# Kernel tuning notes

Measured on AMD Instinct MI355X. Metric: run time of the kernel, lower is better.

Reference implementation:

```python
import jax, jax.numpy as jnp
import numpy as np

N = 15872   # number of predictions (31 * 512)
D = 129     # 128 image features + 1 objectness score
H = 128     # block MLP hidden width
IN = 2 * D + 1  # neighbor feats + main feats + add_info (IoU)
NUM_BLOCKS = 2


def _lin(k, fi, fo):
    return jax.random.normal(k, (fi, fo), jnp.float32) / np.sqrt(fi).astype(np.float32)


def setup_inputs() -> dict:
    key = jax.random.key(0)
    ks = jax.random.split(key, 24)
    # ragged neighborhood structure: mean size 16, exactly E = 16*N edges
    sizes = (np.arange(N) % 31) + 1
    E = int(sizes.sum())  # 253952
    rng = np.random.default_rng(0)
    nbr_idx = rng.integers(0, N, size=E).astype(np.int32)
    self_idx = np.repeat(np.arange(N, dtype=np.int32), sizes)  # sorted segment ids

    inp = {
        "interpolated": jax.random.normal(ks[0], (N, D), jnp.float32),
        "add_info": jax.random.uniform(ks[1], (E, 1), dtype=jnp.float32),
        "neighborhood_sizes": jnp.asarray(sizes, jnp.int32),
        "neighborhoods_indexes": jnp.asarray(nbr_idx),
        "self_indexes": jnp.asarray(self_idx),
    }
    # two (block, output) model pairs
    inp["b0_W1"] = _lin(ks[2], IN, H); inp["b0_b1"] = jnp.zeros((H,), jnp.float32)
    inp["b0_W2"] = _lin(ks[3], H, H);  inp["b0_b2"] = jnp.zeros((H,), jnp.float32)
    inp["b0_Wo"] = _lin(ks[4], H, D); inp["b0_bo"] = jnp.zeros((D,), jnp.float32)
    inp["b1_W1"] = _lin(ks[5], IN, H); inp["b1_b1"] = jnp.zeros((H,), jnp.float32)
    inp["b1_W2"] = _lin(ks[6], H, H);  inp["b1_b2"] = jnp.zeros((H,), jnp.float32)
    inp["b1_Wo"] = _lin(ks[7], H, D); inp["b1_bo"] = jnp.zeros((D,), jnp.float32)
    # final layers: 129 -> 64 -> 1
    inp["f_W1"] = _lin(ks[8], D, 64); inp["f_b1"] = jnp.zeros((64,), jnp.float32)
    inp["f_W2"] = _lin(ks[9], 64, 1); inp["f_b2"] = jnp.zeros((1,), jnp.float32)
    return inp


def _lnms_forward(interpolated, add_info, params, nbr_idx, self_idx):
    # params: list of (W1, b1, W2, b2, Wo, bo) per block, plus (fW1, fb1, fW2, fb2)
    for (W1, b1, W2, b2, Wo, bo) in params[:-1]:
        nbr = interpolated[nbr_idx]    # (E, D) gather of neighbor representations
        main = interpolated[self_idx]  # (E, D) gather of owning prediction
        x = jnp.concatenate([nbr, main, add_info], axis=1)  # (E, 2D+1)
        h = jax.nn.relu(x @ W1 + b1)
        h = jax.nn.relu(h @ W2 + b2)   # (E, H) processed neighborhoods
        # ragged per-neighborhood max pool (segments are contiguous/sorted)
        pooled = jax.ops.segment_max(h, self_idx, num_segments=N,
                                     indices_are_sorted=True)  # (N, H)
        block_output = pooled @ Wo + bo  # (N, D)
        interpolated = interpolated + block_output  # residual scatter-update
    fW1, fb1, fW2, fb2 = params[-1]
    return jax.nn.relu(interpolated @ fW1 + fb1) @ fW2 + fb2  # (N, 1)


def reference(interpolated, add_info,
              b0_W1, b0_b1, b0_W2, b0_b2, b0_Wo, b0_bo,
              b1_W1, b1_b1, b1_W2, b1_b2, b1_Wo, b1_bo,
              f_W1, f_b1, f_W2, f_b2,
              neighborhood_sizes, neighborhoods_indexes, self_indexes):
    params = [
        (b0_W1, b0_b1, b0_W2, b0_b2, b0_Wo, b0_bo),
        (b1_W1, b1_b1, b1_W2, b1_b2, b1_Wo, b1_bo),
        (f_W1, f_b1, f_W2, f_b2),
    ]
    return _lnms_forward(interpolated, add_info, params,
                         neighborhoods_indexes, self_indexes)
```

## Files before the change

### kernel.cpp

```cpp
#include <hip/hip_runtime.h>

#define NSEG 15872
#define DD 129
#define HH 128
#define NTILE (NSEG / 16)

typedef __attribute__((ext_vector_type(8))) short s16x8;
typedef __attribute__((ext_vector_type(4))) float f32x4;

__device__ __forceinline__ unsigned short f2bf(float x) {
  union { float f; unsigned u; } c; c.f = x;
  unsigned r = c.u + 0x7FFFu + ((c.u >> 16) & 1u);
  return (unsigned short)(r >> 16);
}

__global__ __launch_bounds__(256) void scan_sort_kernel(
    const int* __restrict__ sizes, int* __restrict__ offs,
    int* __restrict__ sorted) {
  extern __shared__ int dynS[];
  int* szS = dynS;
  int* tmpS = dynS + NSEG;
  __shared__ int sums[256];
  __shared__ int bins[1024];
  const int t = threadIdx.x;

  for (int i = t; i < NSEG; i += 256) szS[i] = sizes[i];
  for (int i = t; i < 1024; i += 256) bins[i] = 0;
  __syncthreads();

  const int chunk = (NSEG + 255) >> 8;
  const int s0 = t * chunk, s1 = min(s0 + chunk, NSEG);
  int s = 0;
  for (int i = s0; i < s1; ++i) s += szS[i];
  sums[t] = s;
  __syncthreads();
  for (int d = 1; d < 256; d <<= 1) {
    int u = (t >= d) ? sums[t - d] : 0;
    __syncthreads();
    sums[t] += u;
    __syncthreads();
  }
  int a = sums[t] - s;
  for (int i = s0; i < s1; ++i) { tmpS[i] = a; a += szS[i]; }
  __syncthreads();
  for (int i = t; i < NSEG; i += 256) offs[i] = tmpS[i];
  if (t == 255) offs[NSEG] = a;

  for (int i = t; i < NSEG; i += 256) {
    int sz = szS[i]; sz = sz < 0 ? 0 : (sz > 1023 ? 1023 : sz);
    atomicAdd(&bins[sz], 1);
  }
  __syncthreads();
  const int c0 = bins[t * 4], c1 = bins[t * 4 + 1];
  const int c2 = bins[t * 4 + 2], c3 = bins[t * 4 + 3];
  const int loc = c0 + c1 + c2 + c3;
  sums[t] = loc;
  __syncthreads();
  for (int d = 1; d < 256; d <<= 1) {
    int u = (t >= d) ? sums[t - d] : 0;
    __syncthreads();
    sums[t] += u;
    __syncthreads();
  }
  const int base = sums[t] - loc;
  bins[t * 4]     = base;
  bins[t * 4 + 1] = base + c0;
  bins[t * 4 + 2] = base + c0 + c1;
  bins[t * 4 + 3] = base + c0 + c1 + c2;
  __syncthreads();
  for (int i = t; i < NSEG; i += 256) {
    int sz = szS[i]; sz = sz < 0 ? 0 : (sz > 1023 ? 1023 : sz);
    int pos = atomicAdd(&bins[sz], 1);
    tmpS[pos] = i;
  }
  __syncthreads();
  for (int i = t; i < NSEG; i += 256) sorted[i] = tmpS[i];
}

__device__ __forceinline__ void packB8(short* out, int idx8, const float* W,
                                       int N, int ld, int ncols, int kLimit,
                                       int rowBase) {
  const int n = (idx8 >> 3) % N;
  const int g = idx8 / (8 * N);
  s16x8 o;
#pragma unroll
  for (int i = 0; i < 8; ++i) {
    const int row = g * 8 + i;
    float v = 0.f;
    if (row < kLimit && n < ncols) v = W[(long)(rowBase + row) * ld + n];
    o[i] = (short)f2bf(v);
  }
  *(s16x8*)(out + idx8) = o;
}

__device__ __forceinline__ void packB2perm8(short* out, int idx8,
                                            const float* W) {
  const int n = (idx8 >> 3) & 127;
  const int g = idx8 >> 10;
  s16x8 o;
#pragma unroll
  for (int i = 0; i < 8; ++i)
    o[i] = (short)f2bf(W[(long)(i * 16 + g) * HH + n]);
  *(s16x8*)(out + idx8) = o;
}

#define PACK_IDS 161792
#define TAB_IDS (NSEG * 160)
#define PACKV (PACK_IDS / 8)
#define TABV (TAB_IDS / 8)
__global__ __launch_bounds__(256) void pack_tab_kernel(
    const float* __restrict__ interp, unsigned short* __restrict__ tab,
    const float* __restrict__ W1b0, const float* __restrict__ W1b1,
    const float* __restrict__ W2b0, const float* __restrict__ W2b1,
    const float* __restrict__ Wob0, const float* __restrict__ Wob1,
    const float* __restrict__ fW1, short* __restrict__ PB1,
    short* __restrict__ PB2, short* __restrict__ PWo,
    short* __restrict__ PW1m, short* __restrict__ PfW1) {
  int vid = blockIdx.x * 256 + threadIdx.x;
  if (vid < PACKV) {
    int idx = vid * 8;
    if (idx < 40960) {
      packB8(PB1 + (idx / 20480) * 20480, idx % 20480,
             (idx < 20480) ? W1b0 : W1b1, 128, 128, 128, 129, 0);
      return;
    }
    idx -= 40960;
    if (idx < 32768) {
      packB2perm8(PB2 + (idx / 16384) * 16384, idx % 16384,
                  (idx < 16384) ? W2b0 : W2b1);
      return;
    }
    idx -= 32768;
    if (idx < 36864) {
      packB8(PWo + (idx / 18432) * 18432, idx % 18432,
             (idx < 18432) ? Wob0 : Wob1, 144, 129, 129, 128, 0);
      return;
    }
    idx -= 36864;
    if (idx < 40960) {
      packB8(PW1m + (idx / 20480) * 20480, idx % 20480,
             (idx < 20480) ? W1b0 : W1b1, 128, 128, 128, 129, 129);
      return;
    }
    idx -= 40960;
    packB8(PfW1, idx, fW1, 64, 64, 64, 129, 0);
    return;
  }
  vid -= PACKV;
  if (vid < TABV) {
    const int n = vid / 20;
    const int g = vid - n * 20;
    s16x8 o = (s16x8){0, 0, 0, 0, 0, 0, 0, 0};
    if (g < 16) {
      const float* src = interp + (long)n * DD + g * 8;
#pragma unroll
      for (int i = 0; i < 8; ++i) o[i] = (short)f2bf(src[i]);
    } else if (g == 16) {
      o[0] = (short)f2bf(interp[(long)n * DD + 128]);
    }
    *(s16x8*)(tab + (long)vid * 8) = o;
  }
}

__global__ __launch_bounds__(256) void hmprep_kernel(
    const unsigned short* __restrict__ tab, const short* __restrict__ PW1m,
    const float* __restrict__ b1, float* __restrict__ Hm) {
  const int lane = threadIdx.x & 63, w = threadIdx.x >> 6;
  const int lk = lane >> 4, n16 = lane & 15;
  const int tile = blockIdx.x * 4 + w;
  const unsigned short* arow = tab + (long)(tile * 16 + n16) * 160;
  s16x8 A[5];
#pragma unroll
  for (int ks = 0; ks < 5; ++ks) A[ks] = *(const s16x8*)(arow + ks * 32 + lk * 8);
  f32x4 C[8];
#pragma unroll
  for (int nf = 0; nf < 8; ++nf) C[nf] = (f32x4){0.f, 0.f, 0.f, 0.f};
#pragma unroll
  for (int ks = 0; ks < 5; ++ks)
#pragma unroll
    for (int nf = 0; nf < 8; ++nf) {
      const s16x8 b = *(const s16x8*)(PW1m + (((ks * 4 + lk) * 128) + nf * 16 + n16) * 8);
      C[nf] = __builtin_amdgcn_mfma_f32_16x16x32_bf16(A[ks], b, C[nf], 0, 0, 0);
    }
#pragma unroll
  for (int nf = 0; nf < 8; ++nf) {
    const float bv = b1[nf * 16 + n16];
#pragma unroll
    for (int r = 0; r < 4; ++r)
      Hm[(long)(tile * 16 + lk * 4 + r) * HH + nf * 16 + n16] = C[nf][r] + bv;
  }
}

__device__ __forceinline__ int pairEdge(int row, int oLo, int sLo, int oHi,
                                        int sHi) {
  int e = (row < sLo) ? (oLo + row) : (oHi + row - sLo);
  if (row >= sLo + sHi) e = oHi + sHi - 1;
  return e;
}

__global__ __launch_bounds__(512, 2) void edge_kernel(
    const unsigned short* __restrict__ tab, const short* __restrict__ PB1,
    const short* __restrict__ PB2, const float* __restrict__ W1,
    const float* __restrict__ Hm, const float* __restrict__ iou,
    const int* __restrict__ nbrIdx, const int* __restrict__ offs,
    const int* __restrict__ sorted, const float* __restrict__ b2,
    unsigned short* __restrict__ pooled) {
  extern __shared__ __align__(16) char smem[];
  short* Bs1 = (short*)smem;
  short* Bs2 = (short*)(smem + 40960);
  short* stAll = (short*)(smem + 73728);
  {
    const f32x4* s1 = (const f32x4*)PB1;
    f32x4* d1 = (f32x4*)Bs1;
    for (int i = threadIdx.x; i < 2560; i += 512) d1[i] = s1[i];
    const f32x4* s2 = (const f32x4*)PB2;
    f32x4* d2 = (f32x4*)Bs2;
    for (int i = threadIdx.x; i < 2048; i += 512) d2[i] = s2[i];
  }
  __syncthreads();

  const int lane = threadIdx.x & 63;
  const int w = threadIdx.x >> 6;
  const int lk = lane >> 4, n16 = lane & 15;
  short* stA = stAll + w * 2 * (16 * 136);
  short* stB = stA + 16 * 136;

  float wv[8], bv[8];
#pragma unroll
  for (int nf = 0; nf < 8; ++nf) {
    wv[nf] = W1[258 * HH + nf * 16 + n16];
    bv[nf] = b2[nf * 16 + n16];
  }

  const int wid = (blockIdx.x << 3) + w;
  const int nw = gridDim.x << 3;
  const int npairs = NSEG >> 1;

  for (int p = wid; p < npairs; p += 2 * nw) {
    const int pA = p;
    int pB = p + nw;
    if (pB >= npairs) pB = pA;
    const int segLoA = sorted[pA], segHiA = sorted[NSEG - 1 - pA];
    const int segLoB = sorted[pB], segHiB = sorted[NSEG - 1 - pB];
    const int oLoA = offs[segLoA], sLoA = offs[segLoA + 1] - oLoA;
    const int oHiA = offs[segHiA], sHiA = offs[segHiA + 1] - oHiA;
    const int oLoB = offs[segLoB], sLoB = offs[segLoB + 1] - oLoB;
    const int oHiB = offs[segHiB], sHiB = offs[segHiB + 1] - oHiB;
    const int nt = (max(sLoA + sHiA, sLoB + sHiB) + 15) >> 4;

    float hmLoA[8], hmHiA[8], hmLoB[8], hmHiB[8];
    float pmLoA[8], pmHiA[8], pmLoB[8], pmHiB[8];
#pragma unroll
    for (int nf = 0; nf < 8; ++nf) {
      const int col = nf * 16 + n16;
      hmLoA[nf] = Hm[(long)segLoA * HH + col];
      hmHiA[nf] = Hm[(long)segHiA * HH + col];
      hmLoB[nf] = Hm[(long)segLoB * HH + col];
      hmHiB[nf] = Hm[(long)segHiB * HH + col];
      pmLoA[nf] = 0.f; pmHiA[nf] = 0.f; pmLoB[nf] = 0.f; pmHiB[nf] = 0.f;
    }

    for (int t = 0; t < nt; ++t) {
      const int row16 = (t << 4) + n16;
      const int eA = pairEdge(row16, oLoA, sLoA, oHiA, sHiA);
      const int eB = pairEdge(row16, oLoB, sLoB, oHiB, sHiB);
      const unsigned short* rA = tab + (long)nbrIdx[eA] * 160;
      const unsigned short* rB = tab + (long)nbrIdx[eB] * 160;
      s16x8 AA[5], AB[5];
#pragma unroll
      for (int ks = 0; ks < 5; ++ks) {
        AA[ks] = *(const s16x8*)(rA + ks * 32 + lk * 8);
        AB[ks] = *(const s16x8*)(rB + ks * 32 + lk * 8);
      }
      float ioA[4], ioB[4];
#pragma unroll
      for (int r = 0; r < 4; ++r) {
        const int row = (t << 4) + lk * 4 + r;
        ioA[r] = iou[pairEdge(row, oLoA, sLoA, oHiA, sHiA)];
        ioB[r] = iou[pairEdge(row, oLoB, sLoB, oHiB, sHiB)];
      }
      f32x4 C1A[8], C1B[8];
#pragma unroll
      for (int nf = 0; nf < 8; ++nf) {
        C1A[nf] = (f32x4){0.f, 0.f, 0.f, 0.f};
        C1B[nf] = (f32x4){0.f, 0.f, 0.f, 0.f};
      }
#pragma unroll
      for (int ks = 0; ks < 5; ++ks)
#pragma unroll
        for (int nf = 0; nf < 8; ++nf) {
          const s16x8 b = *(const s16x8*)(Bs1 + (((ks * 4 + lk) * 128) + nf * 16 + n16) * 8);
          C1A[nf] = __builtin_amdgcn_mfma_f32_16x16x32_bf16(AA[ks], b, C1A[nf], 0, 0, 0);
          C1B[nf] = __builtin_amdgcn_mfma_f32_16x16x32_bf16(AB[ks], b, C1B[nf], 0, 0, 0);
        }
#pragma unroll
      for (int r = 0; r < 4; ++r) {
        const int row = (t << 4) + lk * 4 + r;
        const bool lA = row < sLoA, lB = row < sLoB;
        s16x8 oA, oB;
#pragma unroll
        for (int nf = 0; nf < 8; ++nf) {
          const float hA = lA ? hmLoA[nf] : hmHiA[nf];
          const float hB = lB ? hmLoB[nf] : hmHiB[nf];
          oA[nf] = (short)f2bf(fmaxf(C1A[nf][r] + ioA[r] * wv[nf] + hA, 0.f));
          oB[nf] = (short)f2bf(fmaxf(C1B[nf][r] + ioB[r] * wv[nf] + hB, 0.f));
        }
        *(s16x8*)(stA + (lk * 4 + r) * 136 + n16 * 8) = oA;
        *(s16x8*)(stB + (lk * 4 + r) * 136 + n16 * 8) = oB;
      }
      s16x8 A2A[4], A2B[4];
#pragma unroll
      for (int ks = 0; ks < 4; ++ks) {
        A2A[ks] = *(const s16x8*)(stA + n16 * 136 + ks * 32 + lk * 8);
        A2B[ks] = *(const s16x8*)(stB + n16 * 136 + ks * 32 + lk * 8);
      }
      f32x4 C2A[8], C2B[8];
#pragma unroll
      for (int nf = 0; nf < 8; ++nf) {
        C2A[nf] = (f32x4){0.f, 0.f, 0.f, 0.f};
        C2B[nf] = (f32x4){0.f, 0.f, 0.f, 0.f};
      }
#pragma unroll
      for (int ks = 0; ks < 4; ++ks)
#pragma unroll
        for (int nf = 0; nf < 8; ++nf) {
          const s16x8 b = *(const s16x8*)(Bs2 + (((ks * 4 + lk) * 128) + nf * 16 + n16) * 8);
          C2A[nf] = __builtin_amdgcn_mfma_f32_16x16x32_bf16(A2A[ks], b, C2A[nf], 0, 0, 0);
          C2B[nf] = __builtin_amdgcn_mfma_f32_16x16x32_bf16(A2B[ks], b, C2B[nf], 0, 0, 0);
        }
#pragma unroll
      for (int r = 0; r < 4; ++r) {
        const int row = (t << 4) + lk * 4 + r;
        const bool lA = row < sLoA, lB = row < sLoB;
#pragma unroll
        for (int nf = 0; nf < 8; ++nf) {
          const float vA = C2A[nf][r] + bv[nf];
          const float vB = C2B[nf][r] + bv[nf];
          if (lA) pmLoA[nf] = fmaxf(pmLoA[nf], vA);
          else    pmHiA[nf] = fmaxf(pmHiA[nf], vA);
          if (lB) pmLoB[nf] = fmaxf(pmLoB[nf], vB);
          else    pmHiB[nf] = fmaxf(pmHiB[nf], vB);
        }
      }
    }
#pragma unroll
    for (int nf = 0; nf < 8; ++nf) {
      float a = pmLoA[nf], b = pmHiA[nf], c = pmLoB[nf], d = pmHiB[nf];
      a = fmaxf(a, __shfl_xor(a, 16, 64)); a = fmaxf(a, __shfl_xor(a, 32, 64));
      b = fmaxf(b, __shfl_xor(b, 16, 64)); b = fmaxf(b, __shfl_xor(b, 32, 64));
      c = fmaxf(c, __shfl_xor(c, 16, 64)); c = fmaxf(c, __shfl_xor(c, 32, 64));
      d = fmaxf(d, __shfl_xor(d, 16, 64)); d = fmaxf(d, __shfl_xor(d, 32, 64));
      pmLoA[nf] = a; pmHiA[nf] = b; pmLoB[nf] = c; pmHiB[nf] = d;
    }
    if (lane < 16) {
#pragma unroll
      for (int nf = 0; nf < 8; ++nf) {
        const int col = nf * 16 + n16;
        pooled[(long)segLoA * HH + col] = f2bf(pmLoA[nf]);
        pooled[(long)segHiA * HH + col] = f2bf(pmHiA[nf]);
        pooled[(long)segLoB * HH + col] = f2bf(pmLoB[nf]);
        pooled[(long)segHiB * HH + col] = f2bf(pmHiB[nf]);
      }
    }
  }
}

template <int NEXT>
__global__ __launch_bounds__(256) void resout_kernel(
    const unsigned short* __restrict__ pooled, const short* __restrict__ PWo,
    const float* __restrict__ bo, const float* __restrict__ resIn,
    float* __restrict__ resOut, unsigned short* __restrict__ tab,
    const short* __restrict__ PW1mN, const float* __restrict__ b1n,
    float* __restrict__ HmOut,
    const short* __restrict__ PfW1, const float* __restrict__ fb1,
    const float* __restrict__ fW2, const float* __restrict__ fb2,
    float* __restrict__ outFinal) {
  __shared__ short stS[4][16 * 168];
  const int lane = threadIdx.x & 63, w = threadIdx.x >> 6;
  const int lk = lane >> 4, n16 = lane & 15;
  short* st = stS[w];

  {
    const int row = lane >> 2, c0 = 129 + (lane & 3) * 8;
#pragma unroll
    for (int i = 0; i < 8; ++i) st[row * 168 + c0 + i] = 0;
  }

  const int tile = blockIdx.x * 4 + w;
  const unsigned short* arow = pooled + (long)(tile * 16 + n16) * HH;
  s16x8 A[4];
#pragma unroll
  for (int ks = 0; ks < 4; ++ks) A[ks] = *(const s16x8*)(arow + ks * 32 + lk * 8);
  f32x4 C[9];
#pragma unroll
  for (int nf = 0; nf < 9; ++nf) C[nf] = (f32x4){0.f, 0.f, 0.f, 0.f};
#pragma unroll
  for (int ks = 0; ks < 4; ++ks)
#pragma unroll
    for (int nf = 0; nf < 9; ++nf) {
      const s16x8 b = *(const s16x8*)(PWo + (((ks * 4 + lk) * 144) + nf * 16 + n16) * 8);
      C[nf] = __builtin_amdgcn_mfma_f32_16x16x32_bf16(A[ks], b, C[nf], 0, 0, 0);
    }

#pragma unroll
  for (int nf = 0; nf < 8; ++nf) {
    const int col = nf * 16 + n16;
    const float bov = bo[col];
#pragma unroll
    for (int r = 0; r < 4; ++r) {
      const int row = lk * 4 + r;
      const long node = tile * 16 + row;
      const float res = resIn[node * DD + col] + bov + C[nf][r];
      if (NEXT) {
        resOut[node * DD + col] = res;
        tab[node * 160 + col] = f2bf(res);
      }
      st[row * 168 + col] = (short)f2bf(res);
    }
  }
  if (n16 == 0) {
#pragma unroll
    for (int r = 0; r < 4; ++r) {
      const int row = lk * 4 + r;
      const long node = tile * 16 + row;
      const float res = resIn[node * DD + 128] + bo[128] + C[8][r];
      if (NEXT) {
        resOut[node * DD + 128] = res;
        tab[node * 160 + 128] = f2bf(res);
      }
      st[row * 168 + 128] = (short)f2bf(res);
    }
  }

  s16x8 A5[5];
#pragma unroll
  for (int ks = 0; ks < 5; ++ks)
    A5[ks] = *(const s16x8*)(st + n16 * 168 + ks * 32 + lk * 8);

  if (NEXT) {
    f32x4 H[8];
#pragma unroll
    for (int nf = 0; nf < 8; ++nf) H[nf] = (f32x4){0.f, 0.f, 0.f, 0.f};
#pragma unroll
    for (int ks = 0; ks < 5; ++ks)
#pragma unroll
      for (int nf = 0; nf < 8; ++nf) {
        const s16x8 b = *(const s16x8*)(PW1mN + (((ks * 4 + lk) * 128) + nf * 16 + n16) * 8);
        H[nf] = __builtin_amdgcn_mfma_f32_16x16x32_bf16(A5[ks], b, H[nf], 0, 0, 0);
      }
#pragma unroll
    for (int nf = 0; nf < 8; ++nf) {
      const float bv = b1n[nf * 16 + n16];
#pragma unroll
      for (int r = 0; r < 4; ++r)
        HmOut[(long)(tile * 16 + lk * 4 + r) * HH + nf * 16 + n16] = H[nf][r] + bv;
    }
  } else {
    f32x4 Ch[4];
#pragma unroll
    for (int nf = 0; nf < 4; ++nf) Ch[nf] = (f32x4){0.f, 0.f, 0.f, 0.f};
#pragma unroll
    for (int ks = 0; ks < 5; ++ks)
#pragma unroll
      for (int nf = 0; nf < 4; ++nf) {
        const s16x8 b = *(const s16x8*)(PfW1 + (((ks * 4 + lk) * 64) + nf * 16 + n16) * 8);
        Ch[nf] = __builtin_amdgcn_mfma_f32_16x16x32_bf16(A5[ks], b, Ch[nf], 0, 0, 0);
      }
    float b1v[4], w2v[4];
#pragma unroll
    for (int nf = 0; nf < 4; ++nf) {
      b1v[nf] = fb1[nf * 16 + n16];
      w2v[nf] = fW2[nf * 16 + n16];
    }
#pragma unroll
    for (int r = 0; r < 4; ++r) {
      float s = 0.f;
#pragma unroll
      for (int nf = 0; nf < 4; ++nf)
        s += fmaxf(Ch[nf][r] + b1v[nf], 0.f) * w2v[nf];
      s += __shfl_xor(s, 1, 64);
      s += __shfl_xor(s, 2, 64);
      s += __shfl_xor(s, 4, 64);
      s += __shfl_xor(s, 8, 64);
      if (n16 == 0) outFinal[tile * 16 + lk * 4 + r] = s + fb2[0];
    }
  }
}

extern "C" void kernel_launch(void* const* d_in, const int* in_sizes, int n_in,
                              void* d_out, int out_size, void* d_ws, size_t ws_size,
                              hipStream_t stream) {
  const float* interp  = (const float*)d_in[0];
  const float* addInfo = (const float*)d_in[1];
  const int* sizes     = (const int*)d_in[2];
  const int* nbrIdx    = (const int*)d_in[3];
  const float* b0W1 = (const float*)d_in[5];
  const float* b0b1 = (const float*)d_in[6];
  const float* b0W2 = (const float*)d_in[7];
  const float* b0b2 = (const float*)d_in[8];
  const float* b0Wo = (const float*)d_in[9];
  const float* b0bo = (const float*)d_in[10];
  const float* b1W1 = (const float*)d_in[11];
  const float* b1b1 = (const float*)d_in[12];
  const float* b1W2 = (const float*)d_in[13];
  const float* b1b2 = (const float*)d_in[14];
  const float* b1Wo = (const float*)d_in[15];
  const float* b1bo = (const float*)d_in[16];
  const float* fW1  = (const float*)d_in[17];
  const float* fb1  = (const float*)d_in[18];
  const float* fW2  = (const float*)d_in[19];
  const float* fb2  = (const float*)d_in[20];

  char* ws = (char*)d_ws;
  int*            offs  = (int*)(ws + 0);
  short*          PB1   = (short*)(ws + 65536);
  short*          PB2   = (short*)(ws + 147456);
  short*          PWo   = (short*)(ws + 212992);
  short*          PW1m  = (short*)(ws + 286720);
  short*          PfW1  = (short*)(ws + 368640);
  unsigned short* TAB   = (unsigned short*)(ws + 393216);
  float*          HM    = (float*)(ws + 5472256);
  unsigned short* POOLED= (unsigned short*)(ws + 13598720);
  float*          RES   = (float*)(ws + 17661952);
  int*            SORTED= (int*)(ws + 25851904);

  scan_sort_kernel<<<1, 256, 2 * NSEG * sizeof(int), stream>>>(sizes, offs,
                                                               SORTED);
  pack_tab_kernel<<<(PACKV + TABV) / 256, 256, 0, stream>>>(
      interp, TAB, b0W1, b1W1, b0W2, b1W2, b0Wo, b1Wo, fW1,
      PB1, PB2, PWo, PW1m, PfW1);

  const size_t e_lds = 40960 + 32768 + 8 * 2 * 16 * 136 * 2;

  hmprep_kernel<<<NTILE / 4, 256, 0, stream>>>(TAB, PW1m, b0b1, HM);
  edge_kernel<<<256, 512, e_lds, stream>>>(TAB, PB1, PB2, b0W1, HM, addInfo,
                                           nbrIdx, offs, SORTED, b0b2, POOLED);
  resout_kernel<1><<<NTILE / 4, 256, 0, stream>>>(
      POOLED, PWo, b0bo, interp, RES, TAB, PW1m + 20480, b1b1, HM,
      nullptr, nullptr, nullptr, nullptr, nullptr);

  edge_kernel<<<256, 512, e_lds, stream>>>(TAB, PB1 + 20480, PB2 + 16384, b1W1,
                                           HM, addInfo, nbrIdx, offs, SORTED,
                                           b1b2, POOLED);
  resout_kernel<0><<<NTILE / 4, 256, 0, stream>>>(
      POOLED, PWo + 18432, b1bo, RES, nullptr, nullptr, nullptr, nullptr,
      nullptr, PfW1, fb1, fW2, fb2, (float*)d_out);
}
```

Measured before the change: 212.8 us.

## Switch edge MLP to 32x32x16 MFMA with transposed layer-1 and rank-5 correction

```diff
diff --git a/kernel.cpp b/kernel.cpp
--- a/kernel.cpp
+++ b/kernel.cpp
@@ -6,12 +6,17 @@
 #define NTILE (NSEG / 16)
 
 typedef __attribute__((ext_vector_type(8))) short s16x8;
+typedef __attribute__((ext_vector_type(4))) short s16x4;
 typedef __attribute__((ext_vector_type(4))) float f32x4;
+typedef __attribute__((ext_vector_type(16))) float f32x16;
 
 __device__ __forceinline__ unsigned short f2bf(float x) {
   union { float f; unsigned u; } c; c.f = x;
   unsigned r = c.u + 0x7FFFu + ((c.u >> 16) & 1u);
   return (unsigned short)(r >> 16);
+}
+__device__ __forceinline__ float bf2f(unsigned short v) {
+  union { unsigned u; float f; } c; c.u = ((unsigned)v) << 16; return c.f;
 }
 
 __global__ __launch_bounds__(256) void scan_sort_kernel(
@@ -93,14 +98,33 @@
   *(s16x8*)(out + idx8) = o;
 }
 
-__device__ __forceinline__ void packB2perm8(short* out, int idx8,
-                                            const float* W) {
-  const int n = (idx8 >> 3) & 127;
-  const int g = idx8 >> 10;
+__device__ __forceinline__ void packA1T8(short* out, int idx8, const float* W1) {
+  const int unit = idx8 >> 3;
+  const int lane = unit & 63;
+  const int blk = unit >> 6;
+  const int Mblk = blk / 10, ks = blk % 10;
+  const int m = Mblk * 32 + (lane & 31);
+  const int k0 = ks * 16 + ((lane >> 5) << 3);
   s16x8 o;
 #pragma unroll
+  for (int i = 0; i < 8; ++i) {
+    const int k = k0 + i;
+    o[i] = (short)((k < DD) ? f2bf(W1[(long)k * HH + m]) : 0);
+  }
+  *(s16x8*)(out + idx8) = o;
+}
+
+__device__ __forceinline__ void packB2T8(short* out, int idx8, const float* W2) {
+  const int unit = idx8 >> 3;
+  const int lane = unit & 63;
+  const int blk = unit >> 6;
+  const int ks = blk >> 2, nb = blk & 3;
+  const int n = nb * 32 + (lane & 31);
+  const int k0 = ks * 16 + ((lane >> 5) << 3);
+  s16x8 o;
+#pragma unroll
   for (int i = 0; i < 8; ++i)
-    o[i] = (short)f2bf(W[(long)(i * 16 + g) * HH + n]);
+    o[i] = (short)f2bf(W2[(long)(k0 + i) * HH + n]);
   *(s16x8*)(out + idx8) = o;
 }
 
@@ -113,21 +137,21 @@
     const float* __restrict__ W1b0, const float* __restrict__ W1b1,
     const float* __restrict__ W2b0, const float* __restrict__ W2b1,
     const float* __restrict__ Wob0, const float* __restrict__ Wob1,
-    const float* __restrict__ fW1, short* __restrict__ PB1,
+    const float* __restrict__ fW1, short* __restrict__ PA1,
     short* __restrict__ PB2, short* __restrict__ PWo,
     short* __restrict__ PW1m, short* __restrict__ PfW1) {
   int vid = blockIdx.x * 256 + threadIdx.x;
   if (vid < PACKV) {
     int idx = vid * 8;
     if (idx < 40960) {
-      packB8(PB1 + (idx / 20480) * 20480, idx % 20480,
-             (idx < 20480) ? W1b0 : W1b1, 128, 128, 128, 129, 0);
+      packA1T8(PA1 + (idx / 20480) * 20480, idx % 20480,
+               (idx < 20480) ? W1b0 : W1b1);
       return;
     }
     idx -= 40960;
     if (idx < 32768) {
-      packB2perm8(PB2 + (idx / 16384) * 16384, idx % 16384,
-                  (idx < 16384) ? W2b0 : W2b1);
+      packB2T8(PB2 + (idx / 16384) * 16384, idx % 16384,
+               (idx < 16384) ? W2b0 : W2b1);
       return;
     }
     idx -= 32768;
@@ -199,19 +223,19 @@
 }
 
 __global__ __launch_bounds__(512, 2) void edge_kernel(
-    const unsigned short* __restrict__ tab, const short* __restrict__ PB1,
+    const unsigned short* __restrict__ tab, const short* __restrict__ PA1,
     const short* __restrict__ PB2, const float* __restrict__ W1,
     const float* __restrict__ Hm, const float* __restrict__ iou,
     const int* __restrict__ nbrIdx, const int* __restrict__ offs,
     const int* __restrict__ sorted, const float* __restrict__ b2,
     unsigned short* __restrict__ pooled) {
   extern __shared__ __align__(16) char smem[];
-  short* Bs1 = (short*)smem;
+  short* As1 = (short*)smem;
   short* Bs2 = (short*)(smem + 40960);
-  short* stAll = (short*)(smem + 73728);
+  short* bnc = (short*)(smem + 73728);
   {
-    const f32x4* s1 = (const f32x4*)PB1;
-    f32x4* d1 = (f32x4*)Bs1;
+    const f32x4* s1 = (const f32x4*)PA1;
+    f32x4* d1 = (f32x4*)As1;
     for (int i = threadIdx.x; i < 2560; i += 512) d1[i] = s1[i];
     const f32x4* s2 = (const f32x4*)PB2;
     f32x4* d2 = (f32x4*)Bs2;
@@ -221,145 +245,114 @@
 
   const int lane = threadIdx.x & 63;
   const int w = threadIdx.x >> 6;
-  const int lk = lane >> 4, n16 = lane & 15;
-  short* stA = stAll + w * 2 * (16 * 136);
-  short* stB = stA + 16 * 136;
-
-  float wv[8], bv[8];
-#pragma unroll
-  for (int nf = 0; nf < 8; ++nf) {
-    wv[nf] = W1[258 * HH + nf * 16 + n16];
-    bv[nf] = b2[nf * 16 + n16];
+  const int half = lane >> 5, n32 = lane & 31;
+  short* bw = bnc + w * (32 * 144);
+
+  float b2v[4], wvT[4];
+#pragma unroll
+  for (int q = 0; q < 4; ++q) {
+    b2v[q] = b2[q * 32 + n32];
+    wvT[q] = W1[258 * HH + q * 32 + n32];
   }
 
   const int wid = (blockIdx.x << 3) + w;
   const int nw = gridDim.x << 3;
   const int npairs = NSEG >> 1;
-
-  for (int p = wid; p < npairs; p += 2 * nw) {
-    const int pA = p;
-    int pB = p + nw;
-    if (pB >= npairs) pB = pA;
-    const int segLoA = sorted[pA], segHiA = sorted[NSEG - 1 - pA];
-    const int segLoB = sorted[pB], segHiB = sorted[NSEG - 1 - pB];
-    const int oLoA = offs[segLoA], sLoA = offs[segLoA + 1] - oLoA;
-    const int oHiA = offs[segHiA], sHiA = offs[segHiA + 1] - oHiA;
-    const int oLoB = offs[segLoB], sLoB = offs[segLoB + 1] - oLoB;
-    const int oHiB = offs[segHiB], sHiB = offs[segHiB + 1] - oHiB;
-    const int nt = (max(sLoA + sHiA, sLoB + sHiB) + 15) >> 4;
-
-    float hmLoA[8], hmHiA[8], hmLoB[8], hmHiB[8];
-    float pmLoA[8], pmHiA[8], pmLoB[8], pmHiB[8];
-#pragma unroll
-    for (int nf = 0; nf < 8; ++nf) {
-      const int col = nf * 16 + n16;
-      hmLoA[nf] = Hm[(long)segLoA * HH + col];
-      hmHiA[nf] = Hm[(long)segHiA * HH + col];
-      hmLoB[nf] = Hm[(long)segLoB * HH + col];
-      hmHiB[nf] = Hm[(long)segHiB * HH + col];
-      pmLoA[nf] = 0.f; pmHiA[nf] = 0.f; pmLoB[nf] = 0.f; pmHiB[nf] = 0.f;
-    }
-
-    for (int t = 0; t < nt; ++t) {
-      const int row16 = (t << 4) + n16;
-      const int eA = pairEdge(row16, oLoA, sLoA, oHiA, sHiA);
-      const int eB = pairEdge(row16, oLoB, sLoB, oHiB, sHiB);
-      const unsigned short* rA = tab + (long)nbrIdx[eA] * 160;
-      const unsigned short* rB = tab + (long)nbrIdx[eB] * 160;
-      s16x8 AA[5], AB[5];
-#pragma unroll
-      for (int ks = 0; ks < 5; ++ks) {
-        AA[ks] = *(const s16x8*)(rA + ks * 32 + lk * 8);
-        AB[ks] = *(const s16x8*)(rB + ks * 32 + lk * 8);
-      }
-      float ioA[4], ioB[4];
-#pragma unroll
-      for (int r = 0; r < 4; ++r) {
-        const int row = (t << 4) + lk * 4 + r;
-        ioA[r] = iou[pairEdge(row, oLoA, sLoA, oHiA, sHiA)];
-        ioB[r] = iou[pairEdge(row, oLoB, sLoB, oHiB, sHiB)];
-      }
-      f32x4 C1A[8], C1B[8];
-#pragma unroll
-      for (int nf = 0; nf < 8; ++nf) {
-        C1A[nf] = (f32x4){0.f, 0.f, 0.f, 0.f};
-        C1B[nf] = (f32x4){0.f, 0.f, 0.f, 0.f};
-      }
-#pragma unroll
-      for (int ks = 0; ks < 5; ++ks)
-#pragma unroll
-        for (int nf = 0; nf < 8; ++nf) {
-          const s16x8 b = *(const s16x8*)(Bs1 + (((ks * 4 + lk) * 128) + nf * 16 + n16) * 8);
-          C1A[nf] = __builtin_amdgcn_mfma_f32_16x16x32_bf16(AA[ks], b, C1A[nf], 0, 0, 0);
-          C1B[nf] = __builtin_amdgcn_mfma_f32_16x16x32_bf16(AB[ks], b, C1B[nf], 0, 0, 0);
+  const short oneBf = (short)0x3F80;
+
+  for (int p = wid; p < npairs; p += nw) {
+    const int segLo = sorted[p], segHi = sorted[NSEG - 1 - p];
+    const int oLo = offs[segLo], sLo = offs[segLo + 1] - oLo;
+    const int oHi = offs[segHi], sHi = offs[segHi + 1] - oHi;
+    const int nchunk = (sLo + sHi + 31) >> 5;
+
+    float mxLo[4], mxHi[4];
+#pragma unroll
+    for (int q = 0; q < 4; ++q) { mxLo[q] = -3.4e38f; mxHi[q] = -3.4e38f; }
+
+    for (int c = 0; c < nchunk; ++c) {
+      const int grow = (c << 5) + n32;
+      const int e = pairEdge(grow, oLo, sLo, oHi, sHi);
+      const unsigned short* ar = tab + (long)nbrIdx[e] * 160;
+      s16x8 X[10];
+#pragma unroll
+      for (int ks = 0; ks < 10; ++ks)
+        X[ks] = *(const s16x8*)(ar + ks * 16 + half * 8);
+      const float io = iou[e];
+      s16x8 bb = (s16x8){0, 0, 0, 0, 0, 0, 0, 0};
+      if (half == 0) {
+        const bool lo = grow < sLo;
+        bb[0] = lo ? oneBf : (short)0;
+        bb[1] = bb[0];
+        bb[2] = lo ? (short)0 : oneBf;
+        bb[3] = bb[2];
+        bb[4] = (short)f2bf(io);
+      }
+
+#pragma unroll
+      for (int Mblk = 0; Mblk < 4; ++Mblk) {
+        f32x16 C;
+#pragma unroll
+        for (int i = 0; i < 16; ++i) C[i] = 0.f;
+#pragma unroll
+        for (int ks = 0; ks < 10; ++ks) {
+          const s16x8 a = *(const s16x8*)(As1 + ((Mblk * 10 + ks) * 64 + lane) * 8);
+          C = __builtin_amdgcn_mfma_f32_32x32x16_bf16(a, X[ks], C, 0, 0, 0);
         }
-#pragma unroll
-      for (int r = 0; r < 4; ++r) {
-        const int row = (t << 4) + lk * 4 + r;
-        const bool lA = row < sLoA, lB = row < sLoB;
-        s16x8 oA, oB;
-#pragma unroll
-        for (int nf = 0; nf < 8; ++nf) {
-          const float hA = lA ? hmLoA[nf] : hmHiA[nf];
-          const float hB = lB ? hmLoB[nf] : hmHiB[nf];
-          oA[nf] = (short)f2bf(fmaxf(C1A[nf][r] + ioA[r] * wv[nf] + hA, 0.f));
-          oB[nf] = (short)f2bf(fmaxf(C1B[nf][r] + ioB[r] * wv[nf] + hB, 0.f));
+        const float hLo = Hm[(long)segLo * HH + Mblk * 32 + n32];
+        const float hHi = Hm[(long)segHi * HH + Mblk * 32 + n32];
+        s16x8 ab = (s16x8){0, 0, 0, 0, 0, 0, 0, 0};
+        if (half == 0) {
+          const unsigned short p0 = f2bf(hLo);
+          ab[0] = (short)p0;
+          ab[1] = (short)f2bf(hLo - bf2f(p0));
+          const unsigned short p1 = f2bf(hHi);
+          ab[2] = (short)p1;
+          ab[3] = (short)f2bf(hHi - bf2f(p1));
+          ab[4] = (short)f2bf(wvT[Mblk]);
         }
-        *(s16x8*)(stA + (lk * 4 + r) * 136 + n16 * 8) = oA;
-        *(s16x8*)(stB + (lk * 4 + r) * 136 + n16 * 8) = oB;
-      }
-      s16x8 A2A[4], A2B[4];
-#pragma unroll
-      for (int ks = 0; ks < 4; ++ks) {
-        A2A[ks] = *(const s16x8*)(stA + n16 * 136 + ks * 32 + lk * 8);
-        A2B[ks] = *(const s16x8*)(stB + n16 * 136 + ks * 32 + lk * 8);
-      }
-      f32x4 C2A[8], C2B[8];
-#pragma unroll
-      for (int nf = 0; nf < 8; ++nf) {
-        C2A[nf] = (f32x4){0.f, 0.f, 0.f, 0.f};
-        C2B[nf] = (f32x4){0.f, 0.f, 0.f, 0.f};
-      }
-#pragma unroll
-      for (int ks = 0; ks < 4; ++ks)
-#pragma unroll
-        for (int nf = 0; nf < 8; ++nf) {
-          const s16x8 b = *(const s16x8*)(Bs2 + (((ks * 4 + lk) * 128) + nf * 16 + n16) * 8);
-          C2A[nf] = __builtin_amdgcn_mfma_f32_16x16x32_bf16(A2A[ks], b, C2A[nf], 0, 0, 0);
-          C2B[nf] = __builtin_amdgcn_mfma_f32_16x16x32_bf16(A2B[ks], b, C2B[nf], 0, 0, 0);
+        C = __builtin_amdgcn_mfma_f32_32x32x16_bf16(ab, bb, C, 0, 0, 0);
+#pragma unroll
+        for (int g = 0; g < 4; ++g) {
+          s16x4 o;
+#pragma unroll
+          for (int j = 0; j < 4; ++j)
+            o[j] = (short)f2bf(fmaxf(C[4 * g + j], 0.f));
+          *(s16x4*)(bw + n32 * 144 + Mblk * 32 + 8 * g + 4 * half) = o;
         }
-#pragma unroll
-      for (int r = 0; r < 4; ++r) {
-        const int row = (t << 4) + lk * 4 + r;
-        const bool lA = row < sLoA, lB = row < sLoB;
-#pragma unroll
-        for (int nf = 0; nf < 8; ++nf) {
-          const float vA = C2A[nf][r] + bv[nf];
-          const float vB = C2B[nf][r] + bv[nf];
-          if (lA) pmLoA[nf] = fmaxf(pmLoA[nf], vA);
-          else    pmHiA[nf] = fmaxf(pmHiA[nf], vA);
-          if (lB) pmLoB[nf] = fmaxf(pmLoB[nf], vB);
-          else    pmHiB[nf] = fmaxf(pmHiB[nf], vB);
+      }
+
+      s16x8 A2[8];
+#pragma unroll
+      for (int ks = 0; ks < 8; ++ks)
+        A2[ks] = *(const s16x8*)(bw + n32 * 144 + ks * 16 + half * 8);
+#pragma unroll
+      for (int nb = 0; nb < 4; ++nb) {
+        f32x16 D;
+#pragma unroll
+        for (int i = 0; i < 16; ++i) D[i] = 0.f;
+#pragma unroll
+        for (int ks = 0; ks < 8; ++ks) {
+          const s16x8 b = *(const s16x8*)(Bs2 + ((ks * 4 + nb) * 64 + lane) * 8);
+          D = __builtin_amdgcn_mfma_f32_32x32x16_bf16(A2[ks], b, D, 0, 0, 0);
         }
-      }
-    }
-#pragma unroll
-    for (int nf = 0; nf < 8; ++nf) {
-      float a = pmLoA[nf], b = pmHiA[nf], c = pmLoB[nf], d = pmHiB[nf];
-      a = fmaxf(a, __shfl_xor(a, 16, 64)); a = fmaxf(a, __shfl_xor(a, 32, 64));
-      b = fmaxf(b, __shfl_xor(b, 16, 64)); b = fmaxf(b, __shfl_xor(b, 32, 64));
-      c = fmaxf(c, __shfl_xor(c, 16, 64)); c = fmaxf(c, __shfl_xor(c, 32, 64));
-      d = fmaxf(d, __shfl_xor(d, 16, 64)); d = fmaxf(d, __shfl_xor(d, 32, 64));
-      pmLoA[nf] = a; pmHiA[nf] = b; pmLoB[nf] = c; pmHiB[nf] = d;
-    }
-    if (lane < 16) {
-#pragma unroll
-      for (int nf = 0; nf < 8; ++nf) {
-        const int col = nf * 16 + n16;
-        pooled[(long)segLoA * HH + col] = f2bf(pmLoA[nf]);
-        pooled[(long)segHiA * HH + col] = f2bf(pmHiA[nf]);
-        pooled[(long)segLoB * HH + col] = f2bf(pmLoB[nf]);
-        pooled[(long)segHiB * HH + col] = f2bf(pmHiB[nf]);
+#pragma unroll
+        for (int reg = 0; reg < 16; ++reg) {
+          const int rrow = (reg & 3) + 8 * (reg >> 2) + 4 * half;
+          const int gr = (c << 5) + rrow;
+          const float v = D[reg];
+          if (gr < sLo) mxLo[nb] = fmaxf(mxLo[nb], v);
+          else          mxHi[nb] = fmaxf(mxHi[nb], v);
+        }
+      }
+    }
+#pragma unroll
+    for (int nb = 0; nb < 4; ++nb) {
+      float lo = fmaxf(mxLo[nb], __shfl_xor(mxLo[nb], 32, 64));
+      float hi = fmaxf(mxHi[nb], __shfl_xor(mxHi[nb], 32, 64));
+      if (half == 0) {
+        pooled[(long)segLo * HH + nb * 32 + n32] = f2bf(fmaxf(lo + b2v[nb], 0.f));
+        pooled[(long)segHi * HH + nb * 32 + n32] = f2bf(fmaxf(hi + b2v[nb], 0.f));
       }
     }
   }
@@ -513,7 +506,7 @@
 
   char* ws = (char*)d_ws;
   int*            offs  = (int*)(ws + 0);
-  short*          PB1   = (short*)(ws + 65536);
+  short*          PA1   = (short*)(ws + 65536);
   short*          PB2   = (short*)(ws + 147456);
   short*          PWo   = (short*)(ws + 212992);
   short*          PW1m  = (short*)(ws + 286720);
@@ -528,18 +521,18 @@
                                                                SORTED);
   pack_tab_kernel<<<(PACKV + TABV) / 256, 256, 0, stream>>>(
       interp, TAB, b0W1, b1W1, b0W2, b1W2, b0Wo, b1Wo, fW1,
-      PB1, PB2, PWo, PW1m, PfW1);
-
-  const size_t e_lds = 40960 + 32768 + 8 * 2 * 16 * 136 * 2;
+      PA1, PB2, PWo, PW1m, PfW1);
+
+  const size_t e_lds = 40960 + 32768 + 8 * 32 * 144 * 2;
 
   hmprep_kernel<<<NTILE / 4, 256, 0, stream>>>(TAB, PW1m, b0b1, HM);
-  edge_kernel<<<256, 512, e_lds, stream>>>(TAB, PB1, PB2, b0W1, HM, addInfo,
+  edge_kernel<<<256, 512, e_lds, stream>>>(TAB, PA1, PB2, b0W1, HM, addInfo,
                                            nbrIdx, offs, SORTED, b0b2, POOLED);
   resout_kernel<1><<<NTILE / 4, 256, 0, stream>>>(
       POOLED, PWo, b0bo, interp, RES, TAB, PW1m + 20480, b1b1, HM,
       nullptr, nullptr, nullptr, nullptr, nullptr);
 
-  edge_kernel<<<256, 512, e_lds, stream>>>(TAB, PB1 + 20480, PB2 + 16384, b1W1,
+  edge_kernel<<<256, 512, e_lds, stream>>>(TAB, PA1 + 20480, PB2 + 16384, b1W1,
                                            HM, addInfo, nbrIdx, offs, SORTED,
                                            b1b2, POOLED);
   resout_kernel<0><<<NTILE / 4, 256, 0, stream>>>(
```

New measurement: 221.0 us. +3.8%, slower.
